# Optimization experiments

Measured on AMD Instinct MI355X. Metric: run time of the kernel, lower is better.

The kernel has to match this reference:

```python
import jax, jax.numpy as jnp
import numpy as np

B, L, D = 4, 4096, 1024
EPS_NORM = 1e-6
EPS_PHAZOR = 1e-5


def setup_inputs() -> dict:
    key = jax.random.key(0)
    ks = jax.random.split(key, 8)
    gain = 0.01 * np.sqrt(2.0 / (D + D))  # xavier_normal_ with gain=0.01 for dim x dim
    inp = {
        "x": jax.random.normal(ks[0], (B, L, D), dtype=jnp.float32),
        "Wz": (jax.random.normal(ks[1], (D, D), dtype=jnp.float32) * gain),
        "bz": jnp.zeros((D,), jnp.float32),
        "Wza": (jax.random.normal(ks[2], (D, D), dtype=jnp.float32) * gain),
        "bza": jnp.zeros((D,), jnp.float32),
        "Wy": (jax.random.normal(ks[3], (D, D), dtype=jnp.float32) * gain),
        "by": jnp.zeros((D,), jnp.float32),
        "Wya": (jax.random.normal(ks[4], (D, D), dtype=jnp.float32) * gain),
        "bya": jnp.zeros((D,), jnp.float32),
        "norm_w": jnp.ones((D,), jnp.float32),
        "lc_re": jax.random.normal(ks[5], (D,), dtype=jnp.float32),  # last_conv_init real part
        "lc_im": jax.random.normal(ks[6], (D,), dtype=jnp.float32),  # last_conv_init imag part
    }
    return inp


def reference(x, Wz, bz, Wza, bza, Wy, by, Wya, bya, norm_w, lc_re, lc_im):
    b, l, d = x.shape
    # phazor_angle_scale = 0.001 ** linspace(0,1,d) (non-trainable buffer)
    scale = jnp.power(jnp.float32(0.001), jnp.linspace(0.0, 1.0, d, dtype=jnp.float32))
    ln_phazor = EPS_PHAZOR + 1j * scale.astype(jnp.complex64)  # (d,) complex64

    # gated input projection: z = fc_z(x) * silu(fc_z_act(x))
    z = (x @ Wz.T + bz) * jax.nn.silu(x @ Wza.T + bza)
    z = z.astype(jnp.complex64)  # (b, l, d)

    # phazor progression exp(l * ln_phazor), (l, d) complex
    t = jnp.arange(l, dtype=jnp.float32)
    phazor_prog = jnp.exp(t[:, None].astype(jnp.complex64) * ln_phazor[None, :])

    # causal diagonal linear recurrence via zero-padded FFT conv along seq
    phazor_fft = jnp.fft.fft(phazor_prog, n=2 * l, axis=0)          # (2l, d)
    z_fft = jnp.fft.fft(z, n=2 * l, axis=1)                          # (b, 2l, d)
    h_inner = jnp.fft.ifft(z_fft * phazor_fft[None], axis=1)[:, :l]  # (b, l, d)

    # carry-in from previous chunk state: last_conv * phazor_prog * exp(ln_phazor)
    last_conv = (lc_re + 1j * lc_im).astype(jnp.complex64)           # (d,)
    h_cross = last_conv[None, None, :] * (phazor_prog * jnp.exp(ln_phazor)[None, :])[None]

    h = (h_inner + h_cross).real  # (b, l, d) float32

    # RMSNorm(h) then gated output projection
    normed = h * jax.lax.rsqrt(jnp.mean(h * h, axis=-1, keepdims=True) + EPS_NORM) * norm_w
    y = (normed @ Wy.T + by) * jax.nn.silu(x @ Wya.T + bya)
    return y
```

## Files before the change

kernel.cpp:

```cpp
#include <hip/hip_runtime.h>

typedef unsigned short u16;
using bf16x8 = __attribute__((ext_vector_type(8))) __bf16;
using f32x4  = __attribute__((ext_vector_type(4))) float;

#define GL_TO_LDS(gp, sp) \
  __builtin_amdgcn_global_load_lds((const __attribute__((address_space(1))) void*)(gp), \
                                   (__attribute__((address_space(3))) void*)(sp), 16, 0, 0)

#define MFMA_BF16 __builtin_amdgcn_mfma_f32_16x16x32_bf16

__device__ __forceinline__ u16 f2bf(float f){
  unsigned u = __builtin_bit_cast(unsigned, f);
  u += 0x7fffu + ((u >> 16) & 1u);
  return (u16)(u >> 16);
}
__device__ __forceinline__ float bf2f(u16 v){
  unsigned u = ((unsigned)v) << 16;
  return __builtin_bit_cast(float, u);
}

constexpr int SB = 4, SL = 4096, SD = 1024;
constexpr int GM = SB * SL, GN = SD, GK = SD;
constexpr int NT = GK / 64;
constexpr int NCHUNK = 64, CH = SL / NCHUNK;
constexpr float EPS_PHAZOR = 1e-5f;
constexpr float LOG2_SCALE = -9.965784284662087f;

__global__ __launch_bounds__(256) void k_convert(
    const float4* __restrict__ x4, const float4* __restrict__ wz4,
    const float4* __restrict__ wza4, const float4* __restrict__ wy4,
    const float4* __restrict__ wya4, u16* __restrict__ xb, u16* __restrict__ wb){
  int gid = blockIdx.x * 256 + threadIdx.x;
  const float4* src; u16* dst;
  if (gid < (GM * GK / 8)){
    src = x4 + (size_t)gid * 2; dst = xb + (size_t)gid * 8;
  } else {
    int g2 = gid - GM * GK / 8;
    int which = g2 >> 17, off = g2 & 0x1ffff;
    const float4* s4 = which == 0 ? wz4 : which == 1 ? wza4 : which == 2 ? wy4 : wya4;
    src = s4 + (size_t)off * 2; dst = wb + (size_t)which * (GK * GN) + (size_t)off * 8;
  }
  float4 a = src[0], b = src[1];
  u16 r[8] = {f2bf(a.x), f2bf(a.y), f2bf(a.z), f2bf(a.w),
              f2bf(b.x), f2bf(b.y), f2bf(b.z), f2bf(b.w)};
  *reinterpret_cast<uint4*>(dst) = *reinterpret_cast<const uint4*>(r);
}


__global__ __launch_bounds__(256, 2) void k_gdual(
    const u16* __restrict__ A, const u16* __restrict__ W0, const u16* __restrict__ W1,
    const float* __restrict__ bias0, const float* __restrict__ bias1,
    u16* __restrict__ out){
  __shared__ u16 sA[8192], sB0[8192], sB1[8192];
  const int tid = threadIdx.x;
  const int w = tid >> 6, ln = tid & 63;
  const int wm = w >> 1, wn = w & 1;
  const int lr = ln & 15, lg = ln >> 4;
  const int lid = blockIdx.x;
  const int swz = (lid & 7) * 128 + (lid >> 3);
  const int bm = swz >> 3, bn = swz & 7;

  size_t soff[4]; int dof[4];
  #pragma unroll
  for (int j = 0; j < 4; ++j){
    int g = j * 256 + tid, r = g >> 3, s = g & 7;
    soff[j] = (size_t)r * GK + (size_t)((s ^ (r & 7)) * 8);
    dof[j] = g * 16;
  }
  const u16* Ab  = A  + (size_t)(bm * 128) * GK;
  const u16* W0b = W0 + (size_t)(bn * 128) * GK;
  const u16* W1b = W1 + (size_t)(bn * 128) * GK;

  f32x4 acc0[4][4] = {}, acc1[4][4] = {};

  for (int t = 0; t < NT; ++t){
    const int k0 = t * 64;
    #pragma unroll
    for (int j = 0; j < 4; ++j){
      GL_TO_LDS(Ab  + soff[j] + k0, (char*)sA  + dof[j]);
      GL_TO_LDS(W0b + soff[j] + k0, (char*)sB0 + dof[j]);
      GL_TO_LDS(W1b + soff[j] + k0, (char*)sB1 + dof[j]);
    }
    __syncthreads();

    bf16x8 a[4][2], b[4][2];
    #pragma unroll
    for (int mf = 0; mf < 4; ++mf){
      const int row = wm * 64 + mf * 16 + lr;
      #pragma unroll
      for (int ks = 0; ks < 2; ++ks)
        a[mf][ks] = *reinterpret_cast<const bf16x8*>(&sA[row * 64 + ((ks * 4 + lg) ^ (row & 7)) * 8]);
    }
    #pragma unroll
    for (int nf = 0; nf < 4; ++nf){
      const int row = wn * 64 + nf * 16 + lr;
      #pragma unroll
      for (int ks = 0; ks < 2; ++ks)
        b[nf][ks] = *reinterpret_cast<const bf16x8*>(&sB0[row * 64 + ((ks * 4 + lg) ^ (row & 7)) * 8]);
    }
    #pragma unroll
    for (int mf = 0; mf < 4; ++mf)
      #pragma unroll
      for (int nf = 0; nf < 4; ++nf){
        acc0[mf][nf] = MFMA_BF16(a[mf][0], b[nf][0], acc0[mf][nf], 0, 0, 0);
        acc0[mf][nf] = MFMA_BF16(a[mf][1], b[nf][1], acc0[mf][nf], 0, 0, 0);
      }
    #pragma unroll
    for (int nf = 0; nf < 4; ++nf){
      const int row = wn * 64 + nf * 16 + lr;
      #pragma unroll
      for (int ks = 0; ks < 2; ++ks)
        b[nf][ks] = *reinterpret_cast<const bf16x8*>(&sB1[row * 64 + ((ks * 4 + lg) ^ (row & 7)) * 8]);
    }
    #pragma unroll
    for (int mf = 0; mf < 4; ++mf)
      #pragma unroll
      for (int nf = 0; nf < 4; ++nf){
        acc1[mf][nf] = MFMA_BF16(a[mf][0], b[nf][0], acc1[mf][nf], 0, 0, 0);
        acc1[mf][nf] = MFMA_BF16(a[mf][1], b[nf][1], acc1[mf][nf], 0, 0, 0);
      }
    __syncthreads();
  }

  #pragma unroll
  for (int nf = 0; nf < 4; ++nf){
    const int col = bn * 128 + wn * 64 + nf * 16 + lr;
    const float bb0 = bias0[col], bb1 = bias1[col];
    #pragma unroll
    for (int mf = 0; mf < 4; ++mf){
      const int rowb = bm * 128 + wm * 64 + mf * 16 + lg * 4;
      f32x4 v0 = acc0[mf][nf], v1 = acc1[mf][nf];
      #pragma unroll
      for (int r = 0; r < 4; ++r){
        float p1 = v1[r] + bb1;
        float sg = p1 / (1.f + __expf(-p1));
        out[(size_t)(rowb + r) * GN + col] = f2bf((v0[r] + bb0) * sg);
      }
    }
  }
}

template<int MODE>
__global__ __launch_bounds__(256, 3) void k_gsingle(
    const u16* __restrict__ A, const u16* __restrict__ W,
    const float* __restrict__ bias, const u16* __restrict__ gate,
    void* __restrict__ outp){
  __shared__ u16 sA[8192], sB[8192];
  const int tid = threadIdx.x;
  const int w = tid >> 6, ln = tid & 63;
  const int wm = w >> 1, wn = w & 1;
  const int lr = ln & 15, lg = ln >> 4;
  const int lid = blockIdx.x;
  const int swz = (lid & 7) * 128 + (lid >> 3);
  const int bm = swz >> 3, bn = swz & 7;

  size_t soff[4]; int dof[4];
  #pragma unroll
  for (int j = 0; j < 4; ++j){
    int g = j * 256 + tid, r = g >> 3, s = g & 7;
    soff[j] = (size_t)r * GK + (size_t)((s ^ (r & 7)) * 8);
    dof[j] = g * 16;
  }
  const u16* Ab = A + (size_t)(bm * 128) * GK;
  const u16* Wb = W + (size_t)(bn * 128) * GK;

  f32x4 acc[4][4] = {};

  for (int t = 0; t < NT; ++t){
    const int k0 = t * 64;
    #pragma unroll
    for (int j = 0; j < 4; ++j){
      GL_TO_LDS(Ab + soff[j] + k0, (char*)sA + dof[j]);
      GL_TO_LDS(Wb + soff[j] + k0, (char*)sB + dof[j]);
    }
    __syncthreads();

    bf16x8 a[4][2], b[4][2];
    #pragma unroll
    for (int mf = 0; mf < 4; ++mf){
      const int row = wm * 64 + mf * 16 + lr;
      #pragma unroll
      for (int ks = 0; ks < 2; ++ks)
        a[mf][ks] = *reinterpret_cast<const bf16x8*>(&sA[row * 64 + ((ks * 4 + lg) ^ (row & 7)) * 8]);
    }
    #pragma unroll
    for (int nf = 0; nf < 4; ++nf){
      const int row = wn * 64 + nf * 16 + lr;
      #pragma unroll
      for (int ks = 0; ks < 2; ++ks)
        b[nf][ks] = *reinterpret_cast<const bf16x8*>(&sB[row * 64 + ((ks * 4 + lg) ^ (row & 7)) * 8]);
    }
    #pragma unroll
    for (int mf = 0; mf < 4; ++mf)
      #pragma unroll
      for (int nf = 0; nf < 4; ++nf){
        acc[mf][nf] = MFMA_BF16(a[mf][0], b[nf][0], acc[mf][nf], 0, 0, 0);
        acc[mf][nf] = MFMA_BF16(a[mf][1], b[nf][1], acc[mf][nf], 0, 0, 0);
      }
    __syncthreads();
  }

  #pragma unroll
  for (int nf = 0; nf < 4; ++nf){
    const int col = bn * 128 + wn * 64 + nf * 16 + lr;
    const float bb = bias[col];
    #pragma unroll
    for (int mf = 0; mf < 4; ++mf){
      const int rowb = bm * 128 + wm * 64 + mf * 16 + lg * 4;
      f32x4 v = acc[mf][nf];
      if constexpr(MODE == 0){
        u16* gout = (u16*)outp;
        #pragma unroll
        for (int r = 0; r < 4; ++r){
          float p = v[r] + bb;
          gout[(size_t)(rowb + r) * GN + col] = f2bf(p / (1.f + __expf(-p)));
        }
      } else {
        float* fout = (float*)outp;
        #pragma unroll
        for (int r = 0; r < 4; ++r){
          float g = bf2f(gate[(size_t)(rowb + r) * GN + col]);
          fout[(size_t)(rowb + r) * GN + col] = (v[r] + bb) * g;
        }
      }
    }
  }
}

__global__ __launch_bounds__(256) void k_scan1(const u16* __restrict__ z, float2* __restrict__ carry){
  const int d = blockIdx.x * 256 + threadIdx.x;
  const int c = blockIdx.y, b = blockIdx.z;
  const float sc = exp2f(LOG2_SCALE * ((float)d * (1.0f / 1023.0f)));
  float si, co; sincosf(sc, &si, &co);
  const float er = expf(EPS_PHAZOR);
  const float rre = er * co, rim = er * si;
  const u16* zp = z + ((size_t)b * SL + (size_t)c * CH) * SD + d;
  float hre = 0.f, him = 0.f;
  #pragma unroll 8
  for (int i = 0; i < CH; i++){
    float zv = bf2f(zp[i * SD]);
    float nr = fmaf(rre, hre, fmaf(-rim, him, zv));
    him = fmaf(rre, him, rim * hre);
    hre = nr;
  }
  carry[(size_t)(b * NCHUNK + c) * SD + d] = make_float2(hre, him);
}

__global__ __launch_bounds__(256) void k_scan2(const float2* __restrict__ carry,
    const float* __restrict__ lcre, const float* __restrict__ lcim, float2* __restrict__ hin){
  const int idx = blockIdx.x * 256 + threadIdx.x;
  const int b = idx >> 10, d = idx & 1023;
  const float sc = exp2f(LOG2_SCALE * ((float)d * (1.0f / 1023.0f)));
  float si, co; sincosf((float)CH * sc, &si, &co);
  const float eC = expf((float)CH * EPS_PHAZOR);
  const float Rre = eC * co, Rim = eC * si;
  float2 cv[NCHUNK];
  const float2* cp = carry + (size_t)b * NCHUNK * SD + d;
  #pragma unroll
  for (int c = 0; c < NCHUNK; c++) cv[c] = cp[(size_t)c * SD];
  float hre = lcre[d], him = lcim[d];
  float2* hp = hin + (size_t)b * NCHUNK * SD + d;
  #pragma unroll
  for (int c = 0; c < NCHUNK; c++){
    hp[(size_t)c * SD] = make_float2(hre, him);
    float nr = fmaf(Rre, hre, fmaf(-Rim, him, cv[c].x));
    him = fmaf(Rre, him, fmaf(Rim, hre, cv[c].y));
    hre = nr;
  }
}

__global__ __launch_bounds__(256) void k_scan3(u16* __restrict__ zh, const float2* __restrict__ hin){
  const int d = blockIdx.x * 256 + threadIdx.x;
  const int c = blockIdx.y, b = blockIdx.z;
  const float sc = exp2f(LOG2_SCALE * ((float)d * (1.0f / 1023.0f)));
  float si, co; sincosf(sc, &si, &co);
  const float er = expf(EPS_PHAZOR);
  const float rre = er * co, rim = er * si;
  float2 h0 = hin[(size_t)(b * NCHUNK + c) * SD + d];
  float hre = h0.x, him = h0.y;
  u16* zp = zh + ((size_t)b * SL + (size_t)c * CH) * SD + d;
  #pragma unroll 8
  for (int i = 0; i < CH; i++){
    float zv = bf2f(zp[i * SD]);
    float nr = fmaf(rre, hre, fmaf(-rim, him, zv));
    him = fmaf(rre, him, rim * hre);
    hre = nr;
    zp[i * SD] = f2bf(hre);
  }
}

__global__ __launch_bounds__(256) void k_rmsnorm(const u16* __restrict__ h,
    const float* __restrict__ nw, u16* __restrict__ outb){
  const int row = blockIdx.x, tid = threadIdx.x;
  const ushort4 hv = reinterpret_cast<const ushort4*>(h + (size_t)row * SD)[tid];
  float v0 = bf2f(hv.x), v1 = bf2f(hv.y), v2 = bf2f(hv.z), v3 = bf2f(hv.w);
  float ss = v0 * v0 + v1 * v1 + v2 * v2 + v3 * v3;
  #pragma unroll
  for (int o = 32; o; o >>= 1) ss += __shfl_down(ss, o, 64);
  __shared__ float red[5];
  const int lane = tid & 63, wid = tid >> 6;
  if (lane == 0) red[wid] = ss;
  __syncthreads();
  if (tid == 0) red[4] = rsqrtf((red[0] + red[1] + red[2] + red[3]) * (1.0f / (float)SD) + 1e-6f);
  __syncthreads();
  const float inv = red[4];
  const float4 w = reinterpret_cast<const float4*>(nw)[tid];
  u16 r[4] = { f2bf(v0 * inv * w.x), f2bf(v1 * inv * w.y),
               f2bf(v2 * inv * w.z), f2bf(v3 * inv * w.w) };
  reinterpret_cast<ushort4*>(outb + (size_t)row * SD)[tid] = *reinterpret_cast<const ushort4*>(r);
}

extern "C" void kernel_launch(void* const* d_in, const int* in_sizes, int n_in,
                              void* d_out, int out_size, void* d_ws, size_t ws_size,
                              hipStream_t stream){
  const float* x    = (const float*)d_in[0];
  const float* Wz   = (const float*)d_in[1];
  const float* bz   = (const float*)d_in[2];
  const float* Wza  = (const float*)d_in[3];
  const float* bza  = (const float*)d_in[4];
  const float* Wy   = (const float*)d_in[5];
  const float* by   = (const float*)d_in[6];
  const float* Wya  = (const float*)d_in[7];
  const float* bya  = (const float*)d_in[8];
  const float* nw   = (const float*)d_in[9];
  const float* lcre = (const float*)d_in[10];
  const float* lcim = (const float*)d_in[11];

  char* ws = (char*)d_ws;
  u16*    xb      = (u16*)(ws);
  u16*    normedb = (u16*)(ws);
  u16*    wb      = (u16*)(ws + (32ull << 20));
  u16*    gy      = (u16*)(ws + (40ull << 20));
  u16*    zb      = (u16*)(ws + (72ull << 20));
  float2* carry   = (float2*)(ws + (104ull << 20));
  float2* hin     = (float2*)(ws + (106ull << 20));
  float*  y       = (float*)d_out;

  const size_t WSZ = (size_t)GK * GN;

  k_convert<<<10240, 256, 0, stream>>>((const float4*)x, (const float4*)Wz, (const float4*)Wza,
                                       (const float4*)Wy, (const float4*)Wya, xb, wb);
  k_gdual<<<1024, 256, 0, stream>>>(xb, wb + 0 * WSZ, wb + 1 * WSZ, bz, bza, zb);
  k_gsingle<0><<<1024, 256, 0, stream>>>(xb, wb + 3 * WSZ, bya, nullptr, gy);
  k_scan1<<<dim3(SD / 256, NCHUNK, SB), 256, 0, stream>>>(zb, carry);
  k_scan2<<<(SB * SD) / 256, 256, 0, stream>>>(carry, lcre, lcim, hin);
  k_scan3<<<dim3(SD / 256, NCHUNK, SB), 256, 0, stream>>>(zb, hin);
  k_rmsnorm<<<GM, 256, 0, stream>>>(zb, nw, normedb);
  k_gsingle<1><<<1024, 256, 0, stream>>>(normedb, wb + 2 * WSZ, by, gy, y);
}
```

Baseline: 335.4 us.

## Fuse RMSNorm and gate GEMM into final dual GEMM with folded norm weights

Removes the standalone RMSNorm kernel and the separate gate GEMM by folding norm_w into Wy columns during conversion and accumulating per-row sum of squares in the scan3 kernel via wave reductions and atomics. The final kernel computes both the Wy GEMM on unnormalized h and the Wya GEMM on x, then applies the rsqrt scale, bias and SiLU gate in the epilogue. This avoids writing and rereading the normalized activations and the gate buffer. In exchange it adds per-row atomics in scan3, and the dual GEMM doubles LDS use, which may lower occupancy. The sum of squares is taken over fp32 h rather than the bf16-rounded values.

Measured after the change: 331.3 us. About the same (-1.2%).

```diff
diff --git a/kernel.cpp b/kernel.cpp
--- a/kernel.cpp
+++ b/kernel.cpp
@@ -30,18 +30,26 @@
 __global__ __launch_bounds__(256) void k_convert(
     const float4* __restrict__ x4, const float4* __restrict__ wz4,
     const float4* __restrict__ wza4, const float4* __restrict__ wy4,
-    const float4* __restrict__ wya4, u16* __restrict__ xb, u16* __restrict__ wb){
+    const float4* __restrict__ wya4, const float4* __restrict__ nw4,
+    u16* __restrict__ xb, u16* __restrict__ wb){
   int gid = blockIdx.x * 256 + threadIdx.x;
   const float4* src; u16* dst;
+  bool scale = false; int off = 0;
   if (gid < (GM * GK / 8)){
     src = x4 + (size_t)gid * 2; dst = xb + (size_t)gid * 8;
   } else {
     int g2 = gid - GM * GK / 8;
-    int which = g2 >> 17, off = g2 & 0x1ffff;
+    int which = g2 >> 17; off = g2 & 0x1ffff;
     const float4* s4 = which == 0 ? wz4 : which == 1 ? wza4 : which == 2 ? wy4 : wya4;
     src = s4 + (size_t)off * 2; dst = wb + (size_t)which * (GK * GN) + (size_t)off * 8;
+    scale = (which == 2);
   }
   float4 a = src[0], b = src[1];
+  if (scale){
+    float4 na = nw4[(off & 127) * 2], nb = nw4[(off & 127) * 2 + 1];
+    a.x *= na.x; a.y *= na.y; a.z *= na.z; a.w *= na.w;
+    b.x *= nb.x; b.y *= nb.y; b.z *= nb.z; b.w *= nb.w;
+  }
   u16 r[8] = {f2bf(a.x), f2bf(a.y), f2bf(a.z), f2bf(a.w),
               f2bf(b.x), f2bf(b.y), f2bf(b.z), f2bf(b.w)};
   *reinterpret_cast<uint4*>(dst) = *reinterpret_cast<const uint4*>(r);
@@ -141,12 +149,12 @@
   }
 }
 
-template<int MODE>
-__global__ __launch_bounds__(256, 3) void k_gsingle(
-    const u16* __restrict__ A, const u16* __restrict__ W,
-    const float* __restrict__ bias, const u16* __restrict__ gate,
-    void* __restrict__ outp){
-  __shared__ u16 sA[8192], sB[8192];
+__global__ __launch_bounds__(256, 2) void k_gfinal(
+    const u16* __restrict__ A0, const u16* __restrict__ A1,
+    const u16* __restrict__ W0, const u16* __restrict__ W1,
+    const float* __restrict__ bias0, const float* __restrict__ bias1,
+    const float* __restrict__ ssq, float* __restrict__ out){
+  __shared__ u16 sA0[8192], sA1[8192], sB0[8192], sB1[8192];
   const int tid = threadIdx.x;
   const int w = tid >> 6, ln = tid & 63;
   const int wm = w >> 1, wn = w & 1;
@@ -162,17 +170,21 @@
     soff[j] = (size_t)r * GK + (size_t)((s ^ (r & 7)) * 8);
     dof[j] = g * 16;
   }
-  const u16* Ab = A + (size_t)(bm * 128) * GK;
-  const u16* Wb = W + (size_t)(bn * 128) * GK;
-
-  f32x4 acc[4][4] = {};
+  const u16* A0b = A0 + (size_t)(bm * 128) * GK;
+  const u16* A1b = A1 + (size_t)(bm * 128) * GK;
+  const u16* W0b = W0 + (size_t)(bn * 128) * GK;
+  const u16* W1b = W1 + (size_t)(bn * 128) * GK;
+
+  f32x4 acc0[4][4] = {}, acc1[4][4] = {};
 
   for (int t = 0; t < NT; ++t){
     const int k0 = t * 64;
     #pragma unroll
     for (int j = 0; j < 4; ++j){
-      GL_TO_LDS(Ab + soff[j] + k0, (char*)sA + dof[j]);
-      GL_TO_LDS(Wb + soff[j] + k0, (char*)sB + dof[j]);
+      GL_TO_LDS(A0b + soff[j] + k0, (char*)sA0 + dof[j]);
+      GL_TO_LDS(A1b + soff[j] + k0, (char*)sA1 + dof[j]);
+      GL_TO_LDS(W0b + soff[j] + k0, (char*)sB0 + dof[j]);
+      GL_TO_LDS(W1b + soff[j] + k0, (char*)sB1 + dof[j]);
     }
     __syncthreads();
 
@@ -182,47 +194,63 @@
       const int row = wm * 64 + mf * 16 + lr;
       #pragma unroll
       for (int ks = 0; ks < 2; ++ks)
-        a[mf][ks] = *reinterpret_cast<const bf16x8*>(&sA[row * 64 + ((ks * 4 + lg) ^ (row & 7)) * 8]);
+        a[mf][ks] = *reinterpret_cast<const bf16x8*>(&sA0[row * 64 + ((ks * 4 + lg) ^ (row & 7)) * 8]);
     }
     #pragma unroll
     for (int nf = 0; nf < 4; ++nf){
       const int row = wn * 64 + nf * 16 + lr;
       #pragma unroll
       for (int ks = 0; ks < 2; ++ks)
-        b[nf][ks] = *reinterpret_cast<const bf16x8*>(&sB[row * 64 + ((ks * 4 + lg) ^ (row & 7)) * 8]);
+        b[nf][ks] = *reinterpret_cast<const bf16x8*>(&sB0[row * 64 + ((ks * 4 + lg) ^ (row & 7)) * 8]);
     }
     #pragma unroll
     for (int mf = 0; mf < 4; ++mf)
       #pragma unroll
       for (int nf = 0; nf < 4; ++nf){
-        acc[mf][nf] = MFMA_BF16(a[mf][0], b[nf][0], acc[mf][nf], 0, 0, 0);
-        acc[mf][nf] = MFMA_BF16(a[mf][1], b[nf][1], acc[mf][nf], 0, 0, 0);
+        acc0[mf][nf] = MFMA_BF16(a[mf][0], b[nf][0], acc0[mf][nf], 0, 0, 0);
+        acc0[mf][nf] = MFMA_BF16(a[mf][1], b[nf][1], acc0[mf][nf], 0, 0, 0);
+      }
+    #pragma unroll
+    for (int mf = 0; mf < 4; ++mf){
+      const int row = wm * 64 + mf * 16 + lr;
+      #pragma unroll
+      for (int ks = 0; ks < 2; ++ks)
+        a[mf][ks] = *reinterpret_cast<const bf16x8*>(&sA1[row * 64 + ((ks * 4 + lg) ^ (row & 7)) * 8]);
+    }
+    #pragma unroll
+    for (int nf = 0; nf < 4; ++nf){
+      const int row = wn * 64 + nf * 16 + lr;
+      #pragma unroll
+      for (int ks = 0; ks < 2; ++ks)
+        b[nf][ks] = *reinterpret_cast<const bf16x8*>(&sB1[row * 64 + ((ks * 4 + lg) ^ (row & 7)) * 8]);
+    }
+    #pragma unroll
+    for (int mf = 0; mf < 4; ++mf)
+      #pragma unroll
+      for (int nf = 0; nf < 4; ++nf){
+        acc1[mf][nf] = MFMA_BF16(a[mf][0], b[nf][0], acc1[mf][nf], 0, 0, 0);
+        acc1[mf][nf] = MFMA_BF16(a[mf][1], b[nf][1], acc1[mf][nf], 0, 0, 0);
       }
     __syncthreads();
   }
 
   #pragma unroll
-  for (int nf = 0; nf < 4; ++nf){
-    const int col = bn * 128 + wn * 64 + nf * 16 + lr;
-    const float bb = bias[col];
-    #pragma unroll
-    for (int mf = 0; mf < 4; ++mf){
-      const int rowb = bm * 128 + wm * 64 + mf * 16 + lg * 4;
-      f32x4 v = acc[mf][nf];
-      if constexpr(MODE == 0){
-        u16* gout = (u16*)outp;
-        #pragma unroll
-        for (int r = 0; r < 4; ++r){
-          float p = v[r] + bb;
-          gout[(size_t)(rowb + r) * GN + col] = f2bf(p / (1.f + __expf(-p)));
-        }
-      } else {
-        float* fout = (float*)outp;
-        #pragma unroll
-        for (int r = 0; r < 4; ++r){
-          float g = bf2f(gate[(size_t)(rowb + r) * GN + col]);
-          fout[(size_t)(rowb + r) * GN + col] = (v[r] + bb) * g;
-        }
+  for (int mf = 0; mf < 4; ++mf){
+    const int rowb = bm * 128 + wm * 64 + mf * 16 + lg * 4;
+    float iv[4];
+    #pragma unroll
+    for (int r = 0; r < 4; ++r)
+      iv[r] = rsqrtf(ssq[rowb + r] * (1.0f / (float)SD) + 1e-6f);
+    #pragma unroll
+    for (int nf = 0; nf < 4; ++nf){
+      const int col = bn * 128 + wn * 64 + nf * 16 + lr;
+      const float bb0 = bias0[col], bb1 = bias1[col];
+      f32x4 v0 = acc0[mf][nf], v1 = acc1[mf][nf];
+      #pragma unroll
+      for (int r = 0; r < 4; ++r){
+        float p1 = v1[r] + bb1;
+        float sg = p1 / (1.f + __expf(-p1));
+        out[(size_t)(rowb + r) * GN + col] = (iv[r] * v0[r] + bb0) * sg;
       }
     }
   }
@@ -270,9 +298,11 @@
   }
 }
 
-__global__ __launch_bounds__(256) void k_scan3(u16* __restrict__ zh, const float2* __restrict__ hin){
+__global__ __launch_bounds__(256) void k_scan3(u16* __restrict__ zh, const float2* __restrict__ hin,
+                                               float* __restrict__ ssq){
   const int d = blockIdx.x * 256 + threadIdx.x;
   const int c = blockIdx.y, b = blockIdx.z;
+  const int ln = threadIdx.x & 63;
   const float sc = exp2f(LOG2_SCALE * ((float)d * (1.0f / 1023.0f)));
   float si, co; sincosf(sc, &si, &co);
   const float er = expf(EPS_PHAZOR);
@@ -280,35 +310,19 @@
   float2 h0 = hin[(size_t)(b * NCHUNK + c) * SD + d];
   float hre = h0.x, him = h0.y;
   u16* zp = zh + ((size_t)b * SL + (size_t)c * CH) * SD + d;
-  #pragma unroll 8
+  const int rowb = b * SL + c * CH;
+  #pragma unroll 4
   for (int i = 0; i < CH; i++){
     float zv = bf2f(zp[i * SD]);
     float nr = fmaf(rre, hre, fmaf(-rim, him, zv));
     him = fmaf(rre, him, rim * hre);
     hre = nr;
     zp[i * SD] = f2bf(hre);
-  }
-}
-
-__global__ __launch_bounds__(256) void k_rmsnorm(const u16* __restrict__ h,
-    const float* __restrict__ nw, u16* __restrict__ outb){
-  const int row = blockIdx.x, tid = threadIdx.x;
-  const ushort4 hv = reinterpret_cast<const ushort4*>(h + (size_t)row * SD)[tid];
-  float v0 = bf2f(hv.x), v1 = bf2f(hv.y), v2 = bf2f(hv.z), v3 = bf2f(hv.w);
-  float ss = v0 * v0 + v1 * v1 + v2 * v2 + v3 * v3;
-  #pragma unroll
-  for (int o = 32; o; o >>= 1) ss += __shfl_down(ss, o, 64);
-  __shared__ float red[5];
-  const int lane = tid & 63, wid = tid >> 6;
-  if (lane == 0) red[wid] = ss;
-  __syncthreads();
-  if (tid == 0) red[4] = rsqrtf((red[0] + red[1] + red[2] + red[3]) * (1.0f / (float)SD) + 1e-6f);
-  __syncthreads();
-  const float inv = red[4];
-  const float4 w = reinterpret_cast<const float4*>(nw)[tid];
-  u16 r[4] = { f2bf(v0 * inv * w.x), f2bf(v1 * inv * w.y),
-               f2bf(v2 * inv * w.z), f2bf(v3 * inv * w.w) };
-  reinterpret_cast<ushort4*>(outb + (size_t)row * SD)[tid] = *reinterpret_cast<const ushort4*>(r);
+    float p = hre * hre;
+    #pragma unroll
+    for (int o = 32; o; o >>= 1) p += __shfl_xor(p, o, 64);
+    if (ln == 0) atomicAdd(&ssq[rowb + i], p);
+  }
 }
 
 extern "C" void kernel_launch(void* const* d_in, const int* in_sizes, int n_in,
@@ -328,24 +342,23 @@
   const float* lcim = (const float*)d_in[11];
 
   char* ws = (char*)d_ws;
-  u16*    xb      = (u16*)(ws);
-  u16*    normedb = (u16*)(ws);
-  u16*    wb      = (u16*)(ws + (32ull << 20));
-  u16*    gy      = (u16*)(ws + (40ull << 20));
-  u16*    zb      = (u16*)(ws + (72ull << 20));
-  float2* carry   = (float2*)(ws + (104ull << 20));
-  float2* hin     = (float2*)(ws + (106ull << 20));
-  float*  y       = (float*)d_out;
+  u16*    xb    = (u16*)(ws);
+  u16*    wb    = (u16*)(ws + (32ull << 20));
+  u16*    zb    = (u16*)(ws + (40ull << 20));
+  float2* carry = (float2*)(ws + (72ull << 20));
+  float2* hin   = (float2*)(ws + (74ull << 20));
+  float*  ssq   = (float*)(ws + (76ull << 20));
+  float*  y     = (float*)d_out;
 
   const size_t WSZ = (size_t)GK * GN;
 
+  hipMemsetAsync(ssq, 0, GM * sizeof(float), stream);
   k_convert<<<10240, 256, 0, stream>>>((const float4*)x, (const float4*)Wz, (const float4*)Wza,
-                                       (const float4*)Wy, (const float4*)Wya, xb, wb);
+                                       (const float4*)Wy, (const float4*)Wya, (const float4*)nw,
+                                       xb, wb);
   k_gdual<<<1024, 256, 0, stream>>>(xb, wb + 0 * WSZ, wb + 1 * WSZ, bz, bza, zb);
-  k_gsingle<0><<<1024, 256, 0, stream>>>(xb, wb + 3 * WSZ, bya, nullptr, gy);
   k_scan1<<<dim3(SD / 256, NCHUNK, SB), 256, 0, stream>>>(zb, carry);
   k_scan2<<<(SB * SD) / 256, 256, 0, stream>>>(carry, lcre, lcim, hin);
-  k_scan3<<<dim3(SD / 256, NCHUNK, SB), 256, 0, stream>>>(zb, hin);
-  k_rmsnorm<<<GM, 256, 0, stream>>>(zb, nw, normedb);
-  k_gsingle<1><<<1024, 256, 0, stream>>>(normedb, wb + 2 * WSZ, by, gy, y);
-}
+  k_scan3<<<dim3(SD / 256, NCHUNK, SB), 256, 0, stream>>>(zb, hin, ssq);
+  k_gfinal<<<1024, 256, 0, stream>>>(zb, xb, wb + 2 * WSZ, wb + 3 * WSZ, by, bya, ssq, y);
+}
```
